# Kernel optimization log

Hardware: AMD Instinct MI355X
Metric: run time of the kernel (lower is better)

The kernel has to match this reference:

```python
import jax, jax.numpy as jnp
import numpy as np

N = 50000
E = 1600000
F_IN = 256
DIMS = 64
N_CLS = 16
R = 8


def glorot(key, shape):
    fan = shape[-2] + shape[-1] if len(shape) >= 2 else shape[-1] * 2
    std = jnp.sqrt(6.0 / fan)
    return jax.random.uniform(key, shape, jnp.float32, -std, std)


def setup_inputs() -> dict:
    key = jax.random.key(0)
    ks = jax.random.split(key, 12)
    x = jax.random.normal(ks[0], (N, F_IN), jnp.float32)
    edge_index = jax.random.randint(ks[1], (2, E), 0, N)
    edge_weight = jax.random.uniform(ks[2], (E,), jnp.float32)
    edge_color = jax.random.randint(ks[3], (E,), 0, R)
    W1 = glorot(ks[4], (R, F_IN, DIMS))
    atten1 = glorot(ks[5], (R, 2 * DIMS))
    root1 = glorot(ks[6], (F_IN, DIMS))
    bias1 = jnp.zeros((DIMS,), jnp.float32)
    W2 = glorot(ks[7], (R, DIMS, N_CLS))
    atten2 = glorot(ks[8], (R, 2 * N_CLS))
    root2 = glorot(ks[9], (DIMS, N_CLS))
    bias2 = jnp.zeros((N_CLS,), jnp.float32)
    return dict(x=x, edge_index=edge_index, edge_weight=edge_weight,
                edge_color=edge_color, W1=W1, atten1=atten1, root1=root1,
                bias1=bias1, W2=W2, atten2=atten2, root2=root2, bias2=bias2)


def wrgat_conv(x, src, dst, ew, ec, W, atten, root, bias):
    # x: [N, f_in]; W: [R, f_in, d]; atten: [R, 2d]
    d = W.shape[-1]
    xr = jnp.einsum('nf,rfd->rnd', x, W)            # [R, N, d] per-relation projection
    xi = xr[ec, dst]                                 # [E, d] dst (x_i)
    xj = xr[ec, src]                                 # [E, d] src (x_j)
    a_i = atten[:, :d][ec]                           # [E, d]
    a_j = atten[:, d:][ec]
    s = jnp.sum(a_i * xi + a_j * xj, axis=-1)        # [E]
    s = jax.nn.leaky_relu(s, 0.2)
    # segment softmax over (relation, destination) groups
    seg = ec * N + dst                               # [E], each edge belongs to one relation
    nseg = R * N
    m = jax.ops.segment_max(s, seg, num_segments=nseg)
    m = jnp.where(jnp.isfinite(m), m, 0.0)           # empty segments -> 0
    e = jnp.exp(s - m[seg])
    denom = jax.ops.segment_sum(e, seg, num_segments=nseg)
    alpha = e / jnp.maximum(denom[seg], 1e-16)
    msg = (alpha * ew)[:, None] * xj                 # [E, d]
    summed = jax.ops.segment_sum(msg, seg, num_segments=nseg).reshape(R, N, d)
    cnt = jax.ops.segment_sum(jnp.ones_like(ew), seg, num_segments=nseg).reshape(R, N, 1)
    out = (summed / jnp.maximum(cnt, 1.0)).sum(axis=0)  # mean aggr per relation, summed over relations
    return out + x @ root + bias


def reference(x, edge_index, edge_weight, edge_color, W1, atten1, root1, bias1,
              W2, atten2, root2, bias2):
    src, dst = edge_index[0], edge_index[1]          # PyG flow source_to_target: x_j=src, x_i=dst
    h = wrgat_conv(x, src, dst, edge_weight, edge_color, W1, atten1, root1, bias1)
    h = jax.nn.relu(h)                               # dropout p=0 -> identity
    h = wrgat_conv(h, src, dst, edge_weight, edge_color, W2, atten2, root2, bias2)
    return jax.nn.log_softmax(h, axis=1)
```

## Files before the change

### kernel.cpp

```cpp
#include <hip/hip_runtime.h>
#include <math.h>

#define N_NODES 50000
#define N_EDGES 1600000
#define F_IN    256
#define DIMS    64
#define N_CLS   16
#define R_REL   8
#define CAP     96

#define PROJ_BLKS 3519
#define CSR_BLKS  3125
#define FRONT_BLKS (PROJ_BLKS + CSR_BLKS)

typedef short bf16x8 __attribute__((ext_vector_type(8)));
typedef float f32x4  __attribute__((ext_vector_type(4)));
typedef unsigned int u32;
typedef const __attribute__((address_space(1))) u32* gas_ptr;
typedef __attribute__((address_space(3))) u32* las_ptr;

__device__ __forceinline__ void async16(const void* g, void* l) {
    __builtin_amdgcn_global_load_lds((gas_ptr)g, (las_ptr)l, 16, 0, 0);
}

__device__ __forceinline__ unsigned short f2bf(float f) {
    unsigned u = __float_as_uint(f);
    unsigned r = (u + 0x7fffu + ((u >> 16) & 1u)) >> 16;
    return (unsigned short)r;
}
__device__ __forceinline__ float bf2f(unsigned short u) {
    return __uint_as_float(((unsigned)u) << 16);
}

__global__ __launch_bounds__(256) void cvt_x_kernel(
        const float* __restrict__ x, ushort* __restrict__ xb) {
    int i4 = blockIdx.x * 256 + threadIdx.x;
    float4 v = ((const float4*)x)[i4];
    ushort4 o;
    o.x = f2bf(v.x); o.y = f2bf(v.y); o.z = f2bf(v.z); o.w = f2bf(v.w);
    ((ushort4*)xb)[i4] = o;
}

__global__ __launch_bounds__(256) void cvt_w_kernel(
        const float* __restrict__ W1, const float* __restrict__ root1,
        ushort* __restrict__ wt1) {
    int idx = blockIdx.x * 256 + threadIdx.x;
    int r = idx >> 14, rem = idx & 16383;
    int n = rem >> 8, k = rem & 255;
    float v = (r < 8) ? W1[((size_t)r * F_IN + k) * DIMS + n]
                      : root1[(size_t)k * DIMS + n];
    wt1[idx] = f2bf(v);
}

#define BM 128
__global__ __launch_bounds__(256, 6) void front_kernel(
        const ushort* __restrict__ xb, const ushort* __restrict__ wt1,
        const float* __restrict__ at1,
        ushort* __restrict__ xr1b, float* __restrict__ hroot,
        float* __restrict__ si1, float* __restrict__ sj1,
        const int* __restrict__ ei, const int* __restrict__ ecol,
        const float* __restrict__ ew, int* __restrict__ fill,
        unsigned long long* __restrict__ rec) {
    __shared__ ushort xs[BM * 64];
    const int bid = blockIdx.x;
    const int t = threadIdx.x;

    int pb = -1, cb = -1;
    if (bid < 2 * CSR_BLKS) { if (bid & 1) cb = bid >> 1; else pb = bid >> 1; }
    else pb = CSR_BLKS + (bid - 2 * CSR_BLKS);

    if (cb >= 0) {
        int idx = cb * 256 + t;
        int2  s2 = ((const int2*)ei)[idx];
        int2  d2 = ((const int2*)(ei + N_EDGES))[idx];
        int2  c2 = ((const int2*)ecol)[idx];
        float2 w2 = ((const float2*)ew)[idx];
        int p0 = atomicAdd(&fill[d2.x], 1);
        int p1 = atomicAdd(&fill[d2.y], 1);
        unsigned long long r0 =
            ((unsigned long long)__float_as_uint(w2.x) << 32)
            | (unsigned)(s2.x | (c2.x << 16));
        unsigned long long r1 =
            ((unsigned long long)__float_as_uint(w2.y) << 32)
            | (unsigned)(s2.y | (c2.y << 16));
        int i0 = (p0 < CAP) ? d2.x * CAP + p0 : N_NODES * CAP;
        int i1 = (p1 < CAP) ? d2.y * CAP + p1 : N_NODES * CAP;
        __builtin_nontemporal_store(r0, &rec[i0]);
        __builtin_nontemporal_store(r1, &rec[i1]);
        return;
    }

    const int r = pb / 391;
    const int node0 = (pb % 391) * BM;
    const ushort* wrow = wt1 + (size_t)r * 64 * 256;

    const int w = t >> 6, lane = t & 63;
    const int lane15 = lane & 15, quad = lane >> 4;
    const int row0 = w * 32 + lane15;
    const int sw0 = row0 & 7;

    f32x4 acc[2][4];
    #pragma unroll
    for (int a = 0; a < 2; ++a)
        #pragma unroll
        for (int b = 0; b < 4; ++b)
            acc[a][b] = (f32x4){0.f, 0.f, 0.f, 0.f};

    for (int s = 0; s < 4; ++s) {
        __syncthreads();
        #pragma unroll
        for (int c = 0; c < 4; ++c) {
            int slot = c * 256 + t;
            int row = slot >> 3, k8p = slot & 7;
            int k8 = k8p ^ (row & 7);
            int node = node0 + row;
            if (node >= N_NODES) node = N_NODES - 1;
            async16(&xb[(size_t)node * 256 + s * 64 + k8 * 8],
                    &xs[(c * 256 + w * 64) * 8]);
        }
        __syncthreads();
        #pragma unroll
        for (int kk = 0; kk < 2; ++kk) {
            int k8 = kk * 4 + quad;
            int aidx = row0 * 64 + ((k8 ^ sw0) << 3);
            bf16x8 a0 = *(const bf16x8*)&xs[aidx];
            bf16x8 a1 = *(const bf16x8*)&xs[aidx + 16 * 64];
            int kg = s * 64 + kk * 32 + quad * 8;
            #pragma unroll
            for (int nt = 0; nt < 4; ++nt) {
                bf16x8 b = *(const bf16x8*)&wrow[(size_t)(nt * 16 + lane15) * 256 + kg];
                acc[0][nt] = __builtin_amdgcn_mfma_f32_16x16x32_bf16(a0, b, acc[0][nt], 0, 0, 0);
                acc[1][nt] = __builtin_amdgcn_mfma_f32_16x16x32_bf16(a1, b, acc[1][nt], 0, 0, 0);
            }
        }
    }

    const float* at = at1 + r * 128;
    #pragma unroll
    for (int mt = 0; mt < 2; ++mt) {
        float pi[4] = {0.f, 0.f, 0.f, 0.f};
        float pj[4] = {0.f, 0.f, 0.f, 0.f};
        #pragma unroll
        for (int nt = 0; nt < 4; ++nt) {
            int gcol = nt * 16 + lane15;
            float ai = 0.f, aj = 0.f;
            if (r < 8) { ai = at[gcol]; aj = at[64 + gcol]; }
            #pragma unroll
            for (int reg = 0; reg < 4; ++reg) {
                float v = acc[mt][nt][reg];
                int grow = node0 + w * 32 + mt * 16 + quad * 4 + reg;
                if (grow < N_NODES) {
                    if (r < 8)
                        xr1b[((size_t)r * N_NODES + grow) * 64 + gcol] = f2bf(v);
                    else
                        hroot[(size_t)grow * 64 + gcol] = v;
                }
                pi[reg] += ai * v;
                pj[reg] += aj * v;
            }
        }
        if (r < 8) {
            #pragma unroll
            for (int reg = 0; reg < 4; ++reg) {
                float s_ = pi[reg], u_ = pj[reg];
                #pragma unroll
                for (int off = 1; off < 16; off <<= 1) {
                    s_ += __shfl_xor(s_, off, 64);
                    u_ += __shfl_xor(u_, off, 64);
                }
                if (lane15 == 0) {
                    int grow = node0 + w * 32 + mt * 16 + quad * 4 + reg;
                    if (grow < N_NODES) {
                        si1[r * N_NODES + grow] = s_;
                        sj1[r * N_NODES + grow] = u_;
                    }
                }
            }
        }
    }
}

__global__ __launch_bounds__(256) void agg1s_kernel(
        const unsigned long long* __restrict__ rec, const int* __restrict__ fill,
        const float* __restrict__ si, const float* __restrict__ sj,
        const ushort* __restrict__ xr1b, const float* __restrict__ hroot,
        const float* __restrict__ bias1, float* __restrict__ h) {
    __shared__ int   esrc[4][CAP];
    __shared__ float ecoef[4][CAP];
    __shared__ float sden[4][8];
    __shared__ int   scnt[4][8];
    __shared__ float ssi[4][8];
    const int t = threadIdx.x;
    const int w = t >> 6, lane = t & 63;
    const int d = blockIdx.x * 4 + w;
    if (lane < 8) {
        sden[w][lane] = 0.f; scnt[w][lane] = 0;
        ssi[w][lane] = si[lane * N_NODES + d];
    }
    const int n = min(fill[d], CAP);
    const int base = d * CAP;
    float ex[2] = {0.f, 0.f}, ww[2] = {0.f, 0.f};
    int cc[2] = {0, 0};
    #pragma unroll
    for (int ii = 0; ii < 2; ++ii) {
        int i = lane + ii * 64;
        if (i < n) {
            unsigned long long rv = rec[base + i];
            int px = (int)(unsigned)rv;
            int s = px & 0xffff, c = (px >> 16) & 0x7fff;
            esrc[w][i] = px;
            float sc = ssi[w][c] + sj[c * N_NODES + s];
            sc = sc > 0.f ? sc : 0.2f * sc;
            float e = __expf(sc);
            ex[ii] = e; cc[ii] = c; ww[ii] = __uint_as_float((unsigned)(rv >> 32));
            atomicAdd(&sden[w][c], e);
            atomicAdd(&scnt[w][c], 1);
        }
    }
    #pragma unroll
    for (int ii = 0; ii < 2; ++ii) {
        int i = lane + ii * 64;
        if (i < n)
            ecoef[w][i] = ex[ii] / fmaxf(sden[w][cc[ii]], 1e-16f)
                          * ww[ii] / (float)scnt[w][cc[ii]];
    }
    const int sub = lane >> 5;
    const int l31 = lane & 31;
    float ax[8] = {0.f,0.f,0.f,0.f,0.f,0.f,0.f,0.f};
    float ay[8] = {0.f,0.f,0.f,0.f,0.f,0.f,0.f,0.f};
    int i0 = 0;
    for (; i0 + 16 <= n; i0 += 16) {
        u32 rv[8]; float cf[8];
        #pragma unroll
        for (int u = 0; u < 8; ++u) {
            int e = i0 + 2 * u + sub;
            int p = esrc[w][e];
            cf[u] = ecoef[w][e];
            int row = (p >> 16) * N_NODES + (p & 0xffff);
            rv[u] = *(const u32*)&xr1b[(size_t)row * 64 + 2 * l31];
        }
        #pragma unroll
        for (int u = 0; u < 8; ++u) {
            ax[u] += cf[u] * bf2f((unsigned short)(rv[u] & 0xffffu));
            ay[u] += cf[u] * bf2f((unsigned short)(rv[u] >> 16));
        }
    }
    for (int e = i0 + sub; e < n; e += 2) {
        int p = esrc[w][e];
        float c = ecoef[w][e];
        int row = (p >> 16) * N_NODES + (p & 0xffff);
        u32 v = *(const u32*)&xr1b[(size_t)row * 64 + 2 * l31];
        ax[0] += c * bf2f((unsigned short)(v & 0xffffu));
        ay[0] += c * bf2f((unsigned short)(v >> 16));
    }
    float sx = ((ax[0] + ax[1]) + (ax[2] + ax[3])) + ((ax[4] + ax[5]) + (ax[6] + ax[7]));
    float sy = ((ay[0] + ay[1]) + (ay[2] + ay[3])) + ((ay[4] + ay[5]) + (ay[6] + ay[7]));
    sx += __shfl_xor(sx, 32, 64);
    sy += __shfl_xor(sy, 32, 64);
    if (sub == 0) {
        float2 hr = *(const float2*)&hroot[(size_t)d * 64 + 2 * l31];
        float2 bi = *(const float2*)&bias1[2 * l31];
        float2 o;
        o.x = fmaxf(sx + hr.x + bi.x, 0.f);
        o.y = fmaxf(sy + hr.y + bi.y, 0.f);
        *(float2*)&h[(size_t)d * 64 + 2 * l31] = o;
    }
}

__global__ __launch_bounds__(256) void proj2_kernel(
        const float* __restrict__ h, const float* __restrict__ W2,
        const float* __restrict__ atten2, ushort* __restrict__ xr2b,
        float* __restrict__ si2, float* __restrict__ sj2) {
    __shared__ float w2sh[8][64][16];
    __shared__ float a2sh[8][32];
    __shared__ float hsh[32][65];
    const int t = threadIdx.x;
    for (int i = t; i < R_REL * DIMS * N_CLS; i += 256)
        w2sh[i >> 10][(i >> 4) & 63][i & 15] = W2[i];
    if (t < R_REL * 2 * N_CLS) a2sh[t >> 5][t & 31] = atten2[t];
    const int node0 = blockIdx.x * 32;
    for (int i = t; i < 32 * 64; i += 256) {
        int nn = i >> 6, kk = i & 63;
        int node = node0 + nn;
        hsh[nn][kk] = (node < N_NODES) ? h[(size_t)node * 64 + kk] : 0.f;
    }
    __syncthreads();
    const int nl = t & 31, r = t >> 5;
    const int node = node0 + nl;
    float acc[16] = {};
    #pragma unroll 4
    for (int k = 0; k < 64; ++k) {
        float hv = hsh[nl][k];
        #pragma unroll
        for (int c = 0; c < 16; ++c) acc[c] += hv * w2sh[r][k][c];
    }
    if (node < N_NODES) {
        float si = 0.f, sj = 0.f;
        size_t base = ((size_t)r * N_NODES + node) * 16;
        #pragma unroll
        for (int c = 0; c < 16; ++c) {
            si += a2sh[r][c] * acc[c];
            sj += a2sh[r][16 + c] * acc[c];
        }
        #pragma unroll
        for (int c4 = 0; c4 < 4; ++c4) {
            ushort4 o;
            o.x = f2bf(acc[c4 * 4 + 0]); o.y = f2bf(acc[c4 * 4 + 1]);
            o.z = f2bf(acc[c4 * 4 + 2]); o.w = f2bf(acc[c4 * 4 + 3]);
            *(ushort4*)&xr2b[base + c4 * 4] = o;
        }
        si2[r * N_NODES + node] = si;
        sj2[r * N_NODES + node] = sj;
    }
}

__global__ __launch_bounds__(256) void agg2s_kernel(
        const unsigned long long* __restrict__ rec, const int* __restrict__ fill,
        const float* __restrict__ si, const float* __restrict__ sj,
        const ushort* __restrict__ xr2b, const float* __restrict__ h,
        const float* __restrict__ root2, const float* __restrict__ bias2,
        float* __restrict__ out) {
    __shared__ float rsh[64][17];
    __shared__ float hsh[4][64];
    __shared__ int   esrc[4][CAP];
    __shared__ float ecoef[4][CAP];
    __shared__ float sden[4][8];
    __shared__ int   scnt[4][8];
    __shared__ float ssi[4][8];
    const int t = threadIdx.x;
    for (int i = t; i < DIMS * N_CLS; i += 256) rsh[i >> 4][i & 15] = root2[i];
    const int w = t >> 6, lane = t & 63;
    const int d = blockIdx.x * 4 + w;
    hsh[w][lane] = h[(size_t)d * 64 + lane];
    if (lane < 8) {
        sden[w][lane] = 0.f; scnt[w][lane] = 0;
        ssi[w][lane] = si[lane * N_NODES + d];
    }
    const int n = min(fill[d], CAP);
    const int base = d * CAP;
    float ex[2] = {0.f, 0.f}, ww[2] = {0.f, 0.f};
    int cc[2] = {0, 0};
    #pragma unroll
    for (int ii = 0; ii < 2; ++ii) {
        int i = lane + ii * 64;
        if (i < n) {
            unsigned long long rv = rec[base + i];
            int px = (int)(unsigned)rv;
            int s = px & 0xffff, c = (px >> 16) & 0x7fff;
            esrc[w][i] = px;
            float sc = ssi[w][c] + sj[c * N_NODES + s];
            sc = sc > 0.f ? sc : 0.2f * sc;
            float e = __expf(sc);
            ex[ii] = e; cc[ii] = c; ww[ii] = __uint_as_float((unsigned)(rv >> 32));
            atomicAdd(&sden[w][c], e);
            atomicAdd(&scnt[w][c], 1);
        }
    }
    #pragma unroll
    for (int ii = 0; ii < 2; ++ii) {
        int i = lane + ii * 64;
        if (i < n)
            ecoef[w][i] = ex[ii] / fmaxf(sden[w][cc[ii]], 1e-16f)
                          * ww[ii] / (float)scnt[w][cc[ii]];
    }
    __syncthreads();
    const int sub = lane >> 4, cd = lane & 15;
    float a0 = 0.f, a1 = 0.f, a2 = 0.f, a3 = 0.f;
    int i = sub;
    for (; i + 12 < n; i += 16) {
        int p0 = esrc[w][i],      p1 = esrc[w][i + 4];
        int p2 = esrc[w][i + 8],  p3 = esrc[w][i + 12];
        float c0 = ecoef[w][i],      c1 = ecoef[w][i + 4];
        float c2 = ecoef[w][i + 8],  c3 = ecoef[w][i + 12];
        int r0 = (p0 >> 16) * N_NODES + (p0 & 0xffff);
        int r1 = (p1 >> 16) * N_NODES + (p1 & 0xffff);
        int r2 = (p2 >> 16) * N_NODES + (p2 & 0xffff);
        int r3 = (p3 >> 16) * N_NODES + (p3 & 0xffff);
        a0 += c0 * bf2f(xr2b[(size_t)r0 * 16 + cd]);
        a1 += c1 * bf2f(xr2b[(size_t)r1 * 16 + cd]);
        a2 += c2 * bf2f(xr2b[(size_t)r2 * 16 + cd]);
        a3 += c3 * bf2f(xr2b[(size_t)r3 * 16 + cd]);
    }
    for (; i < n; i += 4) {
        int p = esrc[w][i];
        int row = (p >> 16) * N_NODES + (p & 0xffff);
        a0 += ecoef[w][i] * bf2f(xr2b[(size_t)row * 16 + cd]);
    }
    float acc = (a0 + a1) + (a2 + a3);
    #pragma unroll
    for (int k0 = 0; k0 < 16; ++k0) {
        int k = sub * 16 + k0;
        acc += hsh[w][k] * rsh[k][cd];
    }
    acc += __shfl_xor(acc, 16, 64);
    acc += __shfl_xor(acc, 32, 64);
    if (sub == 0) {
        acc += bias2[cd];
        float m = acc;
        #pragma unroll
        for (int off = 8; off; off >>= 1) m = fmaxf(m, __shfl_xor(m, off, 16));
        float ex2 = expf(acc - m);
        float ssum = ex2;
        #pragma unroll
        for (int off = 8; off; off >>= 1) ssum += __shfl_xor(ssum, off, 16);
        out[(size_t)d * 16 + cd] = acc - m - logf(ssum);
    }
}

extern "C" void kernel_launch(void* const* d_in, const int* in_sizes, int n_in,
                              void* d_out, int out_size, void* d_ws, size_t ws_size,
                              hipStream_t stream) {
    const float* x     = (const float*)d_in[0];
    const int*   ei    = (const int*)  d_in[1];
    const float* ew    = (const float*)d_in[2];
    const int*   ecol  = (const int*)  d_in[3];
    const float* W1    = (const float*)d_in[4];
    const float* at1   = (const float*)d_in[5];
    const float* root1 = (const float*)d_in[6];
    const float* b1    = (const float*)d_in[7];
    const float* W2    = (const float*)d_in[8];
    const float* at2   = (const float*)d_in[9];
    const float* root2 = (const float*)d_in[10];
    const float* b2    = (const float*)d_in[11];
    float* out = (float*)d_out;
    float* ws  = (float*)d_ws;

    ushort*   xb    = (ushort*)(ws + 0);
    ushort*   wt1   = (ushort*)(ws + 6400000);
    ushort*   xr1b  = (ushort*)(ws + 6480000);
    float*    hroot = ws + 19280000;
    ushort*   xr2b  = (ushort*)(ws + 22480000);
    float*    si1   = ws + 25680000;
    float*    sj1   = ws + 26080000;
    float*    si2   = ws + 26480000;
    float*    sj2   = ws + 26880000;
    int*      fill  = (int*)(ws + 27280000);
    float*    h     = ws + 27330000;
    unsigned long long* rec = (unsigned long long*)(ws + 30530000);

    hipMemsetAsync(fill, 0, (size_t)N_NODES * 4, stream);

    cvt_x_kernel<<<12500, 256, 0, stream>>>(x, xb);
    cvt_w_kernel<<<576, 256, 0, stream>>>(W1, root1, wt1);
    front_kernel<<<FRONT_BLKS, 256, 0, stream>>>(xb, wt1, at1, xr1b, hroot,
                                                 si1, sj1, ei, ecol, ew, fill, rec);
    agg1s_kernel<<<12500, 256, 0, stream>>>(rec, fill, si1, sj1, xr1b, hroot, b1, h);
    proj2_kernel<<<1563, 256, 0, stream>>>(h, W2, at2, xr2b, si2, sj2);
    agg2s_kernel<<<12500, 256, 0, stream>>>(rec, fill, si2, sj2, xr2b, h, root2, b2, out);
}
```

Measured before the change: 391.9 us.

## Fuse layer-2 projection and root term into layer-1 aggregation; merge convert kernels

```diff
diff --git a/kernel.cpp b/kernel.cpp
--- a/kernel.cpp
+++ b/kernel.cpp
@@ -32,24 +32,25 @@
     return __uint_as_float(((unsigned)u) << 16);
 }
 
-__global__ __launch_bounds__(256) void cvt_x_kernel(
-        const float* __restrict__ x, ushort* __restrict__ xb) {
-    int i4 = blockIdx.x * 256 + threadIdx.x;
-    float4 v = ((const float4*)x)[i4];
-    ushort4 o;
-    o.x = f2bf(v.x); o.y = f2bf(v.y); o.z = f2bf(v.z); o.w = f2bf(v.w);
-    ((ushort4*)xb)[i4] = o;
-}
-
-__global__ __launch_bounds__(256) void cvt_w_kernel(
+__global__ __launch_bounds__(256) void cvt_kernel(
+        const float* __restrict__ x, ushort* __restrict__ xb,
         const float* __restrict__ W1, const float* __restrict__ root1,
         ushort* __restrict__ wt1) {
-    int idx = blockIdx.x * 256 + threadIdx.x;
-    int r = idx >> 14, rem = idx & 16383;
-    int n = rem >> 8, k = rem & 255;
-    float v = (r < 8) ? W1[((size_t)r * F_IN + k) * DIMS + n]
-                      : root1[(size_t)k * DIMS + n];
-    wt1[idx] = f2bf(v);
+    const int bid = blockIdx.x, t = threadIdx.x;
+    if (bid < 12500) {
+        int i4 = bid * 256 + t;
+        float4 v = ((const float4*)x)[i4];
+        ushort4 o;
+        o.x = f2bf(v.x); o.y = f2bf(v.y); o.z = f2bf(v.z); o.w = f2bf(v.w);
+        ((ushort4*)xb)[i4] = o;
+    } else {
+        int idx = (bid - 12500) * 256 + t;
+        int r = idx >> 14, rem = idx & 16383;
+        int n = rem >> 8, k = rem & 255;
+        float v = (r < 8) ? W1[((size_t)r * F_IN + k) * DIMS + n]
+                          : root1[(size_t)k * DIMS + n];
+        wt1[idx] = f2bf(v);
+    }
 }
 
 #define BM 128
@@ -180,16 +181,21 @@
     }
 }
 
-__global__ __launch_bounds__(256) void agg1s_kernel(
+__global__ __launch_bounds__(256) void agg1f_kernel(
         const unsigned long long* __restrict__ rec, const int* __restrict__ fill,
         const float* __restrict__ si, const float* __restrict__ sj,
         const ushort* __restrict__ xr1b, const float* __restrict__ hroot,
-        const float* __restrict__ bias1, float* __restrict__ h) {
+        const float* __restrict__ bias1,
+        const float* __restrict__ W2, const float* __restrict__ atten2,
+        const float* __restrict__ root2,
+        ushort* __restrict__ xr2b, float* __restrict__ si2,
+        float* __restrict__ sj2, float* __restrict__ hroot2) {
     __shared__ int   esrc[4][CAP];
     __shared__ float ecoef[4][CAP];
     __shared__ float sden[4][8];
     __shared__ int   scnt[4][8];
     __shared__ float ssi[4][8];
+    __shared__ float hsh[4][64];
     const int t = threadIdx.x;
     const int w = t >> 6, lane = t & 63;
     const int d = blockIdx.x * 4 + w;
@@ -260,78 +266,63 @@
     if (sub == 0) {
         float2 hr = *(const float2*)&hroot[(size_t)d * 64 + 2 * l31];
         float2 bi = *(const float2*)&bias1[2 * l31];
-        float2 o;
-        o.x = fmaxf(sx + hr.x + bi.x, 0.f);
-        o.y = fmaxf(sy + hr.y + bi.y, 0.f);
-        *(float2*)&h[(size_t)d * 64 + 2 * l31] = o;
-    }
-}
-
-__global__ __launch_bounds__(256) void proj2_kernel(
-        const float* __restrict__ h, const float* __restrict__ W2,
-        const float* __restrict__ atten2, ushort* __restrict__ xr2b,
-        float* __restrict__ si2, float* __restrict__ sj2) {
-    __shared__ float w2sh[8][64][16];
-    __shared__ float a2sh[8][32];
-    __shared__ float hsh[32][65];
-    const int t = threadIdx.x;
-    for (int i = t; i < R_REL * DIMS * N_CLS; i += 256)
-        w2sh[i >> 10][(i >> 4) & 63][i & 15] = W2[i];
-    if (t < R_REL * 2 * N_CLS) a2sh[t >> 5][t & 31] = atten2[t];
-    const int node0 = blockIdx.x * 32;
-    for (int i = t; i < 32 * 64; i += 256) {
-        int nn = i >> 6, kk = i & 63;
-        int node = node0 + nn;
-        hsh[nn][kk] = (node < N_NODES) ? h[(size_t)node * 64 + kk] : 0.f;
-    }
-    __syncthreads();
-    const int nl = t & 31, r = t >> 5;
-    const int node = node0 + nl;
-    float acc[16] = {};
-    #pragma unroll 4
+        hsh[w][2 * l31]     = fmaxf(sx + hr.x + bi.x, 0.f);
+        hsh[w][2 * l31 + 1] = fmaxf(sy + hr.y + bi.y, 0.f);
+    }
+    const int r2 = lane >> 3, cp = lane & 7, c0 = cp * 2;
+    float acc0 = 0.f, acc1 = 0.f;
+    #pragma unroll 8
     for (int k = 0; k < 64; ++k) {
-        float hv = hsh[nl][k];
-        #pragma unroll
-        for (int c = 0; c < 16; ++c) acc[c] += hv * w2sh[r][k][c];
-    }
-    if (node < N_NODES) {
-        float si = 0.f, sj = 0.f;
-        size_t base = ((size_t)r * N_NODES + node) * 16;
-        #pragma unroll
-        for (int c = 0; c < 16; ++c) {
-            si += a2sh[r][c] * acc[c];
-            sj += a2sh[r][16 + c] * acc[c];
-        }
-        #pragma unroll
-        for (int c4 = 0; c4 < 4; ++c4) {
-            ushort4 o;
-            o.x = f2bf(acc[c4 * 4 + 0]); o.y = f2bf(acc[c4 * 4 + 1]);
-            o.z = f2bf(acc[c4 * 4 + 2]); o.w = f2bf(acc[c4 * 4 + 3]);
-            *(ushort4*)&xr2b[base + c4 * 4] = o;
-        }
-        si2[r * N_NODES + node] = si;
-        sj2[r * N_NODES + node] = sj;
+        float hv = hsh[w][k];
+        float2 wv = *(const float2*)&W2[((size_t)r2 * 64 + k) * 16 + c0];
+        acc0 += hv * wv.x; acc1 += hv * wv.y;
+    }
+    float sip = atten2[r2 * 32 + c0]      * acc0 + atten2[r2 * 32 + c0 + 1]  * acc1;
+    float sjp = atten2[r2 * 32 + 16 + c0] * acc0 + atten2[r2 * 32 + 17 + c0] * acc1;
+    #pragma unroll
+    for (int off = 1; off < 8; off <<= 1) {
+        sip += __shfl_xor(sip, off, 64);
+        sjp += __shfl_xor(sjp, off, 64);
+    }
+    u32 pk = ((u32)f2bf(acc1) << 16) | (u32)f2bf(acc0);
+    *(u32*)&xr2b[((size_t)r2 * N_NODES + d) * 16 + c0] = pk;
+    if (cp == 0) {
+        si2[r2 * N_NODES + d] = sip;
+        sj2[r2 * N_NODES + d] = sjp;
+    }
+    const int ks = lane >> 3;
+    float r0a = 0.f, r1a = 0.f;
+    #pragma unroll
+    for (int kk = 0; kk < 8; ++kk) {
+        int k = ks * 8 + kk;
+        float hv = hsh[w][k];
+        float2 rv = *(const float2*)&root2[(size_t)k * 16 + c0];
+        r0a += hv * rv.x; r1a += hv * rv.y;
+    }
+    #pragma unroll
+    for (int off = 8; off < 64; off <<= 1) {
+        r0a += __shfl_xor(r0a, off, 64);
+        r1a += __shfl_xor(r1a, off, 64);
+    }
+    if (ks == 0) {
+        float2 o2; o2.x = r0a; o2.y = r1a;
+        *(float2*)&hroot2[(size_t)d * 16 + c0] = o2;
     }
 }
 
 __global__ __launch_bounds__(256) void agg2s_kernel(
         const unsigned long long* __restrict__ rec, const int* __restrict__ fill,
         const float* __restrict__ si, const float* __restrict__ sj,
-        const ushort* __restrict__ xr2b, const float* __restrict__ h,
-        const float* __restrict__ root2, const float* __restrict__ bias2,
-        float* __restrict__ out) {
-    __shared__ float rsh[64][17];
-    __shared__ float hsh[4][64];
+        const ushort* __restrict__ xr2b, const float* __restrict__ hroot2,
+        const float* __restrict__ bias2, float* __restrict__ out) {
     __shared__ int   esrc[4][CAP];
     __shared__ float ecoef[4][CAP];
     __shared__ float sden[4][8];
     __shared__ int   scnt[4][8];
     __shared__ float ssi[4][8];
     const int t = threadIdx.x;
-    for (int i = t; i < DIMS * N_CLS; i += 256) rsh[i >> 4][i & 15] = root2[i];
     const int w = t >> 6, lane = t & 63;
     const int d = blockIdx.x * 4 + w;
-    hsh[w][lane] = h[(size_t)d * 64 + lane];
     if (lane < 8) {
         sden[w][lane] = 0.f; scnt[w][lane] = 0;
         ssi[w][lane] = si[lane * N_NODES + d];
@@ -363,7 +354,6 @@
             ecoef[w][i] = ex[ii] / fmaxf(sden[w][cc[ii]], 1e-16f)
                           * ww[ii] / (float)scnt[w][cc[ii]];
     }
-    __syncthreads();
     const int sub = lane >> 4, cd = lane & 15;
     float a0 = 0.f, a1 = 0.f, a2 = 0.f, a3 = 0.f;
     int i = sub;
@@ -387,15 +377,10 @@
         a0 += ecoef[w][i] * bf2f(xr2b[(size_t)row * 16 + cd]);
     }
     float acc = (a0 + a1) + (a2 + a3);
-    #pragma unroll
-    for (int k0 = 0; k0 < 16; ++k0) {
-        int k = sub * 16 + k0;
-        acc += hsh[w][k] * rsh[k][cd];
-    }
     acc += __shfl_xor(acc, 16, 64);
     acc += __shfl_xor(acc, 32, 64);
     if (sub == 0) {
-        acc += bias2[cd];
+        acc += hroot2[(size_t)d * 16 + cd] + bias2[cd];
         float m = acc;
         #pragma unroll
         for (int off = 8; off; off >>= 1) m = fmaxf(m, __shfl_xor(m, off, 16));
@@ -425,26 +410,25 @@
     float* out = (float*)d_out;
     float* ws  = (float*)d_ws;
 
-    ushort*   xb    = (ushort*)(ws + 0);
-    ushort*   wt1   = (ushort*)(ws + 6400000);
-    ushort*   xr1b  = (ushort*)(ws + 6480000);
-    float*    hroot = ws + 19280000;
-    ushort*   xr2b  = (ushort*)(ws + 22480000);
-    float*    si1   = ws + 25680000;
-    float*    sj1   = ws + 26080000;
-    float*    si2   = ws + 26480000;
-    float*    sj2   = ws + 26880000;
-    int*      fill  = (int*)(ws + 27280000);
-    float*    h     = ws + 27330000;
+    ushort*   xb     = (ushort*)(ws + 0);
+    ushort*   wt1    = (ushort*)(ws + 6400000);
+    ushort*   xr1b   = (ushort*)(ws + 6480000);
+    float*    hroot  = ws + 19280000;
+    ushort*   xr2b   = (ushort*)(ws + 22480000);
+    float*    si1    = ws + 25680000;
+    float*    sj1    = ws + 26080000;
+    float*    si2    = ws + 26480000;
+    float*    sj2    = ws + 26880000;
+    int*      fill   = (int*)(ws + 27280000);
+    float*    hroot2 = ws + 27330000;
     unsigned long long* rec = (unsigned long long*)(ws + 30530000);
 
     hipMemsetAsync(fill, 0, (size_t)N_NODES * 4, stream);
 
-    cvt_x_kernel<<<12500, 256, 0, stream>>>(x, xb);
-    cvt_w_kernel<<<576, 256, 0, stream>>>(W1, root1, wt1);
+    cvt_kernel<<<13076, 256, 0, stream>>>(x, xb, W1, root1, wt1);
     front_kernel<<<FRONT_BLKS, 256, 0, stream>>>(xb, wt1, at1, xr1b, hroot,
                                                  si1, sj1, ei, ecol, ew, fill, rec);
-    agg1s_kernel<<<12500, 256, 0, stream>>>(rec, fill, si1, sj1, xr1b, hroot, b1, h);
-    proj2_kernel<<<1563, 256, 0, stream>>>(h, W2, at2, xr2b, si2, sj2);
-    agg2s_kernel<<<12500, 256, 0, stream>>>(rec, fill, si2, sj2, xr2b, h, root2, b2, out);
-}
+    agg1f_kernel<<<12500, 256, 0, stream>>>(rec, fill, si1, sj1, xr1b, hroot, b1,
+                                            W2, at2, root2, xr2b, si2, sj2, hroot2);
+    agg2s_kernel<<<12500, 256, 0, stream>>>(rec, fill, si2, sj2, xr2b, hroot2, b2, out);
+}
```

Result: slower. 439.0 us (+12.0%).
